# Kernel optimization log

Measured on AMD Instinct MI355X. Metric: run time of the kernel, lower is better.

## Reference

```python
import jax, jax.numpy as jnp
import numpy as np

B, S, T = 256, 1024, 64

def setup_inputs() -> dict:
    key = jax.random.key(0)
    k1, k2, k3, k4, k5 = jax.random.split(key, 5)
    emissions = jax.random.normal(k1, (B, S, T), dtype=jnp.float32)
    tags = jax.random.randint(k2, (B, S), 0, T, dtype=jnp.int64)
    mask = jnp.ones((B, S), dtype=jnp.int32)
    transitions = jax.random.normal(k3, (T, T), dtype=jnp.float32) * 0.1
    start_transitions = jax.random.normal(k4, (T,), dtype=jnp.float32) * 0.1
    end_transitions = jax.random.normal(k5, (T,), dtype=jnp.float32) * 0.1
    return {"emissions": emissions, "tags": tags, "mask": mask,
            "transitions": transitions, "start_transitions": start_transitions,
            "end_transitions": end_transitions}


def _gold_score(emissions, tags, maskf, transitions, start_transitions, end_transitions):
    # emission score at each gold tag: [B, S]
    emit = jnp.take_along_axis(emissions, tags[:, :, None], axis=2)[:, :, 0]
    # transition score between consecutive gold tags: [B, S-1]
    trans = transitions[tags[:, :-1], tags[:, 1:]]
    score = start_transitions[tags[:, 0]] + emit[:, 0]
    score = score + jnp.sum((trans + emit[:, 1:]) * maskf[:, 1:], axis=1)
    last_pos = maskf.astype(jnp.int32).sum(axis=1) - 1           # [B]
    last_tags = jnp.take_along_axis(tags, last_pos[:, None], axis=1)[:, 0]
    return score + end_transitions[last_tags]


def _log_partition(emissions, maskf, transitions, start_transitions, end_transitions):
    alpha0 = start_transitions[None, :] + emissions[:, 0]        # [B, T]

    def step(alpha, xs):
        emit_t, m_t = xs                                         # [B, T], [B]
        # scores[b, i, j] = alpha[b, i] + transitions[i, j] + emit_t[b, j]
        scores = alpha[:, :, None] + transitions[None, :, :] + emit_t[:, None, :]
        new_alpha = jax.nn.logsumexp(scores, axis=1)             # [B, T]
        alpha = jnp.where(m_t[:, None] > 0, new_alpha, alpha)
        return alpha, None

    xs = (jnp.swapaxes(emissions[:, 1:], 0, 1), jnp.swapaxes(maskf[:, 1:], 0, 1))
    alpha, _ = jax.lax.scan(step, alpha0, xs)
    return jax.nn.logsumexp(alpha + end_transitions[None, :], axis=1)  # [B]


def reference(emissions, tags, mask, transitions, start_transitions, end_transitions):
    maskf = mask.astype(emissions.dtype)
    log_Z = _log_partition(emissions, maskf, transitions, start_transitions, end_transitions)
    score = _gold_score(emissions, tags, maskf, transitions, start_transitions, end_transitions)
    return jnp.mean(log_Z - score)
```

## Files before the change

### kernel.cpp

```cpp
#include <hip/hip_runtime.h>

#define Bn 256
#define Sn 1024
#define Tn 64
#define NCH 16
#define BURN 64
#define SLAB 4
#define RAWSTR 260
#define CROW 72
#define MROW 129
#define LN2 0.69314718055994531f
#define L7LN2 4.8520302639196169f

typedef __attribute__((ext_vector_type(8))) short short8;
typedef __attribute__((ext_vector_type(4))) float f32x4;

__device__ __forceinline__ unsigned short f2bf_rne(float f) {
  unsigned u = __float_as_uint(f);
  u = (u + 0x7fffu + ((u >> 16) & 1u)) >> 16;
  return (unsigned short)u;
}
__device__ __forceinline__ unsigned pk2(float hi, float lo) {
  return __builtin_amdgcn_perm(__float_as_uint(hi), __float_as_uint(lo), 0x07060302);
}
__device__ __forceinline__ unsigned pke(float a, float b) {
  return (unsigned)f2bf_rne(__expf(a - L7LN2)) |
         ((unsigned)f2bf_rne(__expf(b - L7LN2)) << 16);
}
__device__ __forceinline__ short8 cat4(uint2 a, uint2 b) {
  union { unsigned u[4]; short8 s; } x;
  x.u[0] = a.x; x.u[1] = a.y; x.u[2] = b.x; x.u[3] = b.y;
  return x.s;
}
__device__ __forceinline__ void gl_lds16(const void* src, void* dst) {
  __builtin_amdgcn_global_load_lds(
      (const __attribute__((address_space(1))) void*)src,
      (__attribute__((address_space(3))) void*)dst, 16, 0, 0);
}
__device__ __forceinline__ void gl_lds4(const void* src, void* dst) {
  __builtin_amdgcn_global_load_lds(
      (const __attribute__((address_space(1))) void*)src,
      (__attribute__((address_space(3))) void*)dst, 4, 0, 0);
}

__global__ __launch_bounds__(128, 1) void crf_scan(
    const float* __restrict__ em, const int* __restrict__ tags,
    const int* __restrict__ mask, const float* __restrict__ trans,
    const float* __restrict__ startt, const float* __restrict__ endt,
    float* __restrict__ wsL, float* __restrict__ wsGold,
    int* __restrict__ wsM, float* __restrict__ wsSE, float* __restrict__ wsA,
    int* __restrict__ cnt, float* __restrict__ out) {
  const int g = blockIdx.x & 15;
  const int c = blockIdx.x >> 4;
  const int Wc = (c == 0) ? 0 : BURN;
  const int Lc = (c == NCH - 1) ? 63 : 64;
  const int TOT = Wc + Lc;
  const int NSLAB = (TOT + SLAB - 1) / SLAB;
  const int t0 = 64 * c + 1;
  const int tstart = t0 - Wc;
  const int tid = threadIdx.x;
  const int wid = tid >> 6;
  const int lane = tid & 63;
  const int m = lane & 15;
  const int q = lane >> 4;
  const int mrow = 8 * (m >> 2) + (m & 3);

  __shared__ __align__(16) float rawS[3][16 * RAWSTR];
  __shared__ __align__(16) short convS[2][SLAB * 16 * CROW];
  __shared__ int maskL[16 * MROW];
  __shared__ int lastF;
  __shared__ float eend[64];
  __shared__ float rsum[2];

  short8 a00, a01, a10, a11, a20, a21, a30, a31;
  uint2 st0, st1, st2, st3;
  float Slog = 0.f;
  int K = 0, NL = 0;
  const f32x4 zero4 = {0.f, 0.f, 0.f, 0.f};

  auto issue_slab = [&](int s) {
    if (s >= NSLAB) return;
    float* dstb = rawS[s % 3];
    const int rem = TOT - 4 * s;
    if (rem >= SLAB) {
      for (int mm = 0; mm < 16; ++mm)
        gl_lds16(em + ((size_t)(16 * g + mm) * Sn + tstart + 4 * s) * 64 + lane * 4,
                 dstb + mm * RAWSTR);
    } else {
      for (int mm = 0; mm < 16; ++mm)
        for (int u = 0; u < rem; ++u)
          gl_lds4(em + ((size_t)(16 * g + mm) * Sn + tstart + 4 * s + u) * 64 + lane,
                  dstb + mm * RAWSTR + u * 64);
    }
  };
  auto conv_u = [&](const float* rp, short* cb, int mm, int base, int u) {
    float4 v0 = *(const float4*)(rp + u * 64 + 0);
    float4 v1 = *(const float4*)(rp + u * 64 + 4);
    float4 v2 = *(const float4*)(rp + u * 64 + 8);
    float4 v3 = *(const float4*)(rp + u * 64 + 12);
    uint4 o0, o1;
    o0.x = pke(v0.x, v0.y); o0.y = pke(v0.z, v0.w);
    o1.x = pke(v1.x, v1.y); o1.y = pke(v1.z, v1.w);
    o0.z = pke(v2.x, v2.y); o0.w = pke(v2.z, v2.w);
    o1.z = pke(v3.x, v3.y); o1.w = pke(v3.z, v3.w);
    short* cw = cb + (u * 16 + mm) * CROW + base;
    *(uint4*)(cw) = o0;
    *(uint4*)(cw + 16) = o1;
  };
  auto convert_full = [&](int s) {
    const int mm = lane & 15, seg = lane >> 4;
    const float* rp = rawS[s % 3] + mm * RAWSTR + seg * 16;
    short* cb = convS[s & 1];
    const int base = (seg >> 1) * 32 + (seg & 1) * 8;
    #pragma unroll
    for (int u = 0; u < SLAB; ++u) conv_u(rp, cb, mm, base, u);
  };
  auto convert_tail = [&](int s) {
    if (s >= NSLAB) return;
    const int mm = lane & 15, seg = lane >> 4;
    const float* rp = rawS[s % 3] + mm * RAWSTR + seg * 16;
    short* cb = convS[s & 1];
    const int base = (seg >> 1) * 32 + (seg & 1) * 8;
    const int vu = min(SLAB, TOT - 4 * s);
    for (int u = 0; u < vu; ++u) conv_u(rp, cb, mm, base, u);
  };

  if (wid == 0) {
#define LOADA(tm, kc, dst) { \
    _Pragma("unroll") for (int jj = 0; jj < 8; ++jj) { \
      int kk = kc * 32 + q * 8 + jj; \
      dst[jj] = (short)f2bf_rne(__expf(trans[kk * Tn + (32 * ((tm) >> 1) + 4 * ((tm) & 1) + mrow)])); \
    } }
    LOADA(0, 0, a00) LOADA(0, 1, a01) LOADA(1, 0, a10) LOADA(1, 1, a11)
    LOADA(2, 0, a20) LOADA(2, 1, a21) LOADA(3, 0, a30) LOADA(3, 1, a31)
#undef LOADA
    if (c == 0) {
#define INIT0(off, ss) { \
      float4 sv = *(const float4*)(startt + (off)); \
      float4 ev = *(const float4*)(em + (size_t)(16 * g + m) * Sn * Tn + (off)); \
      ss.x = (unsigned)f2bf_rne(__expf(sv.x + ev.x)) | \
             ((unsigned)f2bf_rne(__expf(sv.y + ev.y)) << 16); \
      ss.y = (unsigned)f2bf_rne(__expf(sv.z + ev.z)) | \
             ((unsigned)f2bf_rne(__expf(sv.w + ev.w)) << 16); }
      INIT0(8 * q, st0) INIT0(8 * q + 4, st1)
      INIT0(32 + 8 * q, st2) INIT0(36 + 8 * q, st3)
#undef INIT0
    } else {
      st0.x = 0x3F803F80u; st0.y = 0x3F803F80u; st1 = st0; st2 = st0; st3 = st0;
    }
    issue_slab(0);
    issue_slab(1);
    asm volatile("s_waitcnt vmcnt(0)" ::: "memory");
  } else {
    for (int mm = 0; mm < 16; ++mm) {
      gl_lds4(mask + (size_t)(16 * g + mm) * Sn + tstart + lane,
              (void*)(maskL + mm * MROW));
      bool special = (c == NCH - 1) && (g == 15) && (mm == 15);
      if (!special)
        gl_lds4(mask + (size_t)(16 * g + mm) * Sn + tstart + 64 + lane,
                (void*)(maskL + mm * MROW + 64));
    }
    {
      const int bm = 16 * g + m;
      const int qq = q;
      const int* tg = tags + (size_t)bm * Sn;
      const int* mkb = mask + (size_t)bm * Sn;
      const float* emb = em + (size_t)bm * Sn * Tn;
      float acc = 0.f;
      int cntg = 0;
      #pragma unroll 4
      for (int i = 0; i < 16; ++i) {
        int t = t0 + qq + 4 * i;
        bool ok = t < t0 + Lc;
        int ts = ok ? t : t0;
        int mv = mkb[ts];
        int tp = tg[ts - 1], tc = tg[ts];
        float w = trans[tp * Tn + tc] + emb[(size_t)ts * Tn + tc];
        acc += (ok && mv) ? w : 0.f;
        cntg += ok ? mv : 0;
      }
      acc += __shfl_xor(acc, 16); acc += __shfl_xor(acc, 32);
      cntg += __shfl_xor(cntg, 16); cntg += __shfl_xor(cntg, 32);
      if (qq == 0) { wsGold[c * 256 + bm] = acc; wsM[c * 256 + bm] = cntg; }
    }
    if (c == NCH - 1 && g == 15) {
      int t = tstart + 64 + lane;
      if (t < Sn) maskL[15 * MROW + 64 + lane] = mask[(size_t)255 * Sn + t];
    }
    asm volatile("s_waitcnt vmcnt(0) lgkmcnt(0)" ::: "memory");
  }
  __syncthreads();

  if (wid == 0) {
    issue_slab(2);
    asm volatile("s_waitcnt vmcnt(0)" ::: "memory");
  } else {
    convert_full(0);
    asm volatile("s_waitcnt lgkmcnt(0)" ::: "memory");
  }
  __syncthreads();

#define UNP(ss, x0, x1, x2, x3) \
  x0 = __uint_as_float(ss.x << 16); x1 = __uint_as_float(ss.x & 0xffff0000u); \
  x2 = __uint_as_float(ss.y << 16); x3 = __uint_as_float(ss.y & 0xffff0000u);

  auto renorm = [&](int ttz) {
    float x00, x01, x02, x03, x10, x11, x12, x13;
    float x20, x21, x22, x23, x30, x31, x32, x33;
    UNP(st0, x00, x01, x02, x03) UNP(st1, x10, x11, x12, x13)
    UNP(st2, x20, x21, x22, x23) UNP(st3, x30, x31, x32, x33)
    float sm = (((x00 + x01) + (x02 + x03)) + ((x10 + x11) + (x12 + x13)))
             + (((x20 + x21) + (x22 + x23)) + ((x30 + x31) + (x32 + x33)));
    sm += __shfl_xor(sm, 16); sm += __shfl_xor(sm, 32);
    if (c != 0 && ttz == BURN) { Slog = __logf(sm); K = 0; NL = 0; }
    int k = 127 - (int)((__float_as_uint(sm) >> 23) & 255u);
    float fk = __uint_as_float((unsigned)(127 + k) << 23);
    x00 *= fk; x01 *= fk; x02 *= fk; x03 *= fk;
    x10 *= fk; x11 *= fk; x12 *= fk; x13 *= fk;
    x20 *= fk; x21 *= fk; x22 *= fk; x23 *= fk;
    x30 *= fk; x31 *= fk; x32 *= fk; x33 *= fk;
    st0.x = pk2(x01, x00); st0.y = pk2(x03, x02);
    st1.x = pk2(x11, x10); st1.y = pk2(x13, x12);
    st2.x = pk2(x21, x20); st2.y = pk2(x23, x22);
    st3.x = pk2(x31, x30); st3.y = pk2(x33, x32);
    K += k;
  };

  auto scan_step = [&](const short* ep, int tt) {
    uint2 eu0 = *(const uint2*)(ep + 0 + 4 * q);
    uint2 eu1 = *(const uint2*)(ep + 16 + 4 * q);
    uint2 eu2 = *(const uint2*)(ep + 32 + 4 * q);
    uint2 eu3 = *(const uint2*)(ep + 48 + 4 * q);
    int mv = maskL[m * MROW + tt];
    short8 b0 = cat4(st0, st1);
    short8 b1 = cat4(st2, st3);
    f32x4 d0 = __builtin_amdgcn_mfma_f32_16x16x32_bf16(a00, b0, zero4, 0, 0, 0);
    f32x4 d1 = __builtin_amdgcn_mfma_f32_16x16x32_bf16(a10, b0, zero4, 0, 0, 0);
    f32x4 d2 = __builtin_amdgcn_mfma_f32_16x16x32_bf16(a20, b0, zero4, 0, 0, 0);
    f32x4 d3 = __builtin_amdgcn_mfma_f32_16x16x32_bf16(a30, b0, zero4, 0, 0, 0);
    d0 = __builtin_amdgcn_mfma_f32_16x16x32_bf16(a01, b1, d0, 0, 0, 0);
    d1 = __builtin_amdgcn_mfma_f32_16x16x32_bf16(a11, b1, d1, 0, 0, 0);
    d2 = __builtin_amdgcn_mfma_f32_16x16x32_bf16(a21, b1, d2, 0, 0, 0);
    d3 = __builtin_amdgcn_mfma_f32_16x16x32_bf16(a31, b1, d3, 0, 0, 0);
    const bool live = (mv != 0);
#define EPI(dd, eu, ss) { \
    float e0 = __uint_as_float(eu.x << 16); \
    float e1 = __uint_as_float(eu.x & 0xffff0000u); \
    float e2 = __uint_as_float(eu.y << 16); \
    float e3 = __uint_as_float(eu.y & 0xffff0000u); \
    unsigned nx = pk2(dd[1] * e1, dd[0] * e0); \
    unsigned ny = pk2(dd[3] * e3, dd[2] * e2); \
    ss.x = live ? nx : ss.x; \
    ss.y = live ? ny : ss.y; }
    EPI(d0, eu0, st0) EPI(d1, eu1, st1) EPI(d2, eu2, st2) EPI(d3, eu3, st3)
#undef EPI
    NL += (live && tt >= Wc) ? 1 : 0;
  };

  const int RT = (TOT - 4) >> 2;
  for (int r = 0; r < NSLAB; ++r) {
    if (wid == 0) {
      issue_slab(r + 3);
      if ((r & 1) == 0) renorm(4 * r);
      const short* cbase = convS[r & 1];
      if (r < RT) {
        #pragma unroll
        for (int u = 0; u < SLAB; ++u)
          scan_step(cbase + (u * 16 + m) * CROW, 4 * r + u);
      } else {
        #pragma unroll
        for (int u = 0; u < SLAB; ++u)
          if (4 * r + u < TOT)
            scan_step(cbase + (u * 16 + m) * CROW, 4 * r + u);
      }
      if (r + 3 < NSLAB) asm volatile("s_waitcnt vmcnt(16)" ::: "memory");
      else               asm volatile("s_waitcnt vmcnt(0)" ::: "memory");
    } else {
      if (r < RT) convert_full(r + 1);
      else        convert_tail(r + 1);
      asm volatile("s_waitcnt lgkmcnt(0)" ::: "memory");
    }
    __builtin_amdgcn_s_barrier();
    asm volatile("" ::: "memory");
  }

  if (wid == 0) {
    float x00, x01, x02, x03, x10, x11, x12, x13;
    float x20, x21, x22, x23, x30, x31, x32, x33;
    UNP(st0, x00, x01, x02, x03) UNP(st1, x10, x11, x12, x13)
    UNP(st2, x20, x21, x22, x23) UNP(st3, x30, x31, x32, x33)
    float sm = (((x00 + x01) + (x02 + x03)) + ((x10 + x11) + (x12 + x13)))
             + (((x20 + x21) + (x22 + x23)) + ((x30 + x31) + (x32 + x33)));
    sm += __shfl_xor(sm, 16); sm += __shfl_xor(sm, 32);
    const int bm = 16 * g + m;
    float L = __logf(sm) - Slog + LN2 * (float)(7 * NL - K);
    if (q == 0) wsL[c * 256 + bm] = L;
    if (c == NCH - 1) {
      if (q == 0) wsSE[bm] = __logf(sm);
      wsA[(8 * q + 0) * 256 + bm] = x00;  wsA[(8 * q + 1) * 256 + bm] = x01;
      wsA[(8 * q + 2) * 256 + bm] = x02;  wsA[(8 * q + 3) * 256 + bm] = x03;
      wsA[(8 * q + 4) * 256 + bm] = x10;  wsA[(8 * q + 5) * 256 + bm] = x11;
      wsA[(8 * q + 6) * 256 + bm] = x12;  wsA[(8 * q + 7) * 256 + bm] = x13;
      wsA[(32 + 8 * q + 0) * 256 + bm] = x20; wsA[(32 + 8 * q + 1) * 256 + bm] = x21;
      wsA[(32 + 8 * q + 2) * 256 + bm] = x22; wsA[(32 + 8 * q + 3) * 256 + bm] = x23;
      wsA[(36 + 8 * q + 0) * 256 + bm] = x30; wsA[(36 + 8 * q + 1) * 256 + bm] = x31;
      wsA[(36 + 8 * q + 2) * 256 + bm] = x32; wsA[(36 + 8 * q + 3) * 256 + bm] = x33;
    }
  }
#undef UNP

  __threadfence();
  __syncthreads();
  if (tid == 0) lastF = (atomicAdd(cnt, 1) == 255) ? 1 : 0;
  __syncthreads();
  if (lastF) {
    __threadfence();
    if (tid < 64) eend[tid] = __expf(endt[tid]);
    __syncthreads();
    float vsum = 0.f;
    for (int bb = tid; bb < Bn; bb += 128) {
      float sumL = 0.f, gold = 0.f;
      int msum = 0;
      #pragma unroll
      for (int cc = 0; cc < NCH; ++cc) {
        sumL += wsL[cc * 256 + bb];
        gold += wsGold[cc * 256 + bb];
        msum += wsM[cc * 256 + bb];
      }
      msum += mask[(size_t)bb * Sn];
      float se = 0.f;
      for (int jj = 0; jj < Tn; ++jj) se += wsA[jj * 256 + bb] * eend[jj];
      float logZ = sumL + __logf(se) - wsSE[bb];
      int tg0 = tags[(size_t)bb * Sn];
      int lastTag = tags[(size_t)bb * Sn + (msum - 1)];
      gold += startt[tg0] + em[(size_t)bb * Sn * Tn + tg0] + endt[lastTag];
      vsum += logZ - gold;
    }
    #pragma unroll
    for (int o = 32; o > 0; o >>= 1) vsum += __shfl_xor(vsum, o, 64);
    if (lane == 0) rsum[wid] = vsum;
    __syncthreads();
    if (tid == 0) out[0] = (rsum[0] + rsum[1]) * (1.0f / Bn);
  }
}

extern "C" void kernel_launch(void* const* d_in, const int* in_sizes, int n_in,
                              void* d_out, int out_size, void* d_ws, size_t ws_size,
                              hipStream_t stream) {
  const float* em     = (const float*)d_in[0];
  const int*   tags   = (const int*)d_in[1];
  const int*   mask   = (const int*)d_in[2];
  const float* trans  = (const float*)d_in[3];
  const float* startt = (const float*)d_in[4];
  const float* endt   = (const float*)d_in[5];
  float* out = (float*)d_out;

  float* wsL    = (float*)d_ws;
  float* wsGold = wsL + NCH * 256;
  int*   wsM    = (int*)(wsGold + NCH * 256);
  float* wsSE   = (float*)(wsM + NCH * 256);
  float* wsA    = wsSE + 256;
  int*   cnt    = (int*)(wsA + 64 * 256);

  hipMemsetAsync(cnt, 0, sizeof(int), stream);
  crf_scan<<<256, 128, 0, stream>>>(em, tags, mask, trans, startt, endt,
                                    wsL, wsGold, wsM, wsSE, wsA, cnt, out);
}
```

Before: 169.5 us.

## Split CRF scan block into four specialized waves for load, convert and scan

Raises the block from 2 to 4 wavefronts. Wave 0 only runs the MFMA scan, wave 3 issues the global-to-LDS slab loads, and waves 1 and 2 each convert half of every slab to bf16. The raw buffer goes from triple to double buffering because prefetch now runs one slab ahead on its own wave. The aim is to take load issue and conversion off the scan wave's critical path, at the cost of full __syncthreads per slab across more waves and a shallower prefetch depth.

```diff
diff --git a/kernel.cpp b/kernel.cpp
--- a/kernel.cpp
+++ b/kernel.cpp
@@ -43,7 +43,7 @@
       (__attribute__((address_space(3))) void*)dst, 4, 0, 0);
 }
 
-__global__ __launch_bounds__(128, 1) void crf_scan(
+__global__ __launch_bounds__(256, 1) void crf_scan(
     const float* __restrict__ em, const int* __restrict__ tags,
     const int* __restrict__ mask, const float* __restrict__ trans,
     const float* __restrict__ startt, const float* __restrict__ endt,
@@ -65,12 +65,12 @@
   const int q = lane >> 4;
   const int mrow = 8 * (m >> 2) + (m & 3);
 
-  __shared__ __align__(16) float rawS[3][16 * RAWSTR];
+  __shared__ __align__(16) float rawS[2][16 * RAWSTR];
   __shared__ __align__(16) short convS[2][SLAB * 16 * CROW];
   __shared__ int maskL[16 * MROW];
   __shared__ int lastF;
   __shared__ float eend[64];
-  __shared__ float rsum[2];
+  __shared__ float rsum[4];
 
   short8 a00, a01, a10, a11, a20, a21, a30, a31;
   uint2 st0, st1, st2, st3;
@@ -80,7 +80,7 @@
 
   auto issue_slab = [&](int s) {
     if (s >= NSLAB) return;
-    float* dstb = rawS[s % 3];
+    float* dstb = rawS[s & 1];
     const int rem = TOT - 4 * s;
     if (rem >= SLAB) {
       for (int mm = 0; mm < 16; ++mm)
@@ -107,22 +107,23 @@
     *(uint4*)(cw) = o0;
     *(uint4*)(cw + 16) = o1;
   };
-  auto convert_full = [&](int s) {
+  auto convert2 = [&](int s, int ua) {
     const int mm = lane & 15, seg = lane >> 4;
-    const float* rp = rawS[s % 3] + mm * RAWSTR + seg * 16;
+    const float* rp = rawS[s & 1] + mm * RAWSTR + seg * 16;
     short* cb = convS[s & 1];
     const int base = (seg >> 1) * 32 + (seg & 1) * 8;
-    #pragma unroll
-    for (int u = 0; u < SLAB; ++u) conv_u(rp, cb, mm, base, u);
-  };
-  auto convert_tail = [&](int s) {
+    conv_u(rp, cb, mm, base, ua);
+    conv_u(rp, cb, mm, base, ua + 1);
+  };
+  auto convert_tail2 = [&](int s, int ua) {
     if (s >= NSLAB) return;
     const int mm = lane & 15, seg = lane >> 4;
-    const float* rp = rawS[s % 3] + mm * RAWSTR + seg * 16;
+    const float* rp = rawS[s & 1] + mm * RAWSTR + seg * 16;
     short* cb = convS[s & 1];
     const int base = (seg >> 1) * 32 + (seg & 1) * 8;
     const int vu = min(SLAB, TOT - 4 * s);
-    for (int u = 0; u < vu; ++u) conv_u(rp, cb, mm, base, u);
+    const int ub = min(vu, ua + 2);
+    for (int u = ua; u < ub; ++u) conv_u(rp, cb, mm, base, u);
   };
 
   if (wid == 0) {
@@ -148,10 +149,7 @@
     } else {
       st0.x = 0x3F803F80u; st0.y = 0x3F803F80u; st1 = st0; st2 = st0; st3 = st0;
     }
-    issue_slab(0);
-    issue_slab(1);
-    asm volatile("s_waitcnt vmcnt(0)" ::: "memory");
-  } else {
+  } else if (wid == 1) {
     for (int mm = 0; mm < 16; ++mm) {
       gl_lds4(mask + (size_t)(16 * g + mm) * Sn + tstart + lane,
               (void*)(maskL + mm * MROW));
@@ -160,44 +158,42 @@
         gl_lds4(mask + (size_t)(16 * g + mm) * Sn + tstart + 64 + lane,
                 (void*)(maskL + mm * MROW + 64));
     }
-    {
-      const int bm = 16 * g + m;
-      const int qq = q;
-      const int* tg = tags + (size_t)bm * Sn;
-      const int* mkb = mask + (size_t)bm * Sn;
-      const float* emb = em + (size_t)bm * Sn * Tn;
-      float acc = 0.f;
-      int cntg = 0;
-      #pragma unroll 4
-      for (int i = 0; i < 16; ++i) {
-        int t = t0 + qq + 4 * i;
-        bool ok = t < t0 + Lc;
-        int ts = ok ? t : t0;
-        int mv = mkb[ts];
-        int tp = tg[ts - 1], tc = tg[ts];
-        float w = trans[tp * Tn + tc] + emb[(size_t)ts * Tn + tc];
-        acc += (ok && mv) ? w : 0.f;
-        cntg += ok ? mv : 0;
-      }
-      acc += __shfl_xor(acc, 16); acc += __shfl_xor(acc, 32);
-      cntg += __shfl_xor(cntg, 16); cntg += __shfl_xor(cntg, 32);
-      if (qq == 0) { wsGold[c * 256 + bm] = acc; wsM[c * 256 + bm] = cntg; }
-    }
     if (c == NCH - 1 && g == 15) {
       int t = tstart + 64 + lane;
       if (t < Sn) maskL[15 * MROW + 64 + lane] = mask[(size_t)255 * Sn + t];
     }
     asm volatile("s_waitcnt vmcnt(0) lgkmcnt(0)" ::: "memory");
+  } else if (wid == 2) {
+    const int bm = 16 * g + m;
+    const int qq = q;
+    const int* tg = tags + (size_t)bm * Sn;
+    const int* mkb = mask + (size_t)bm * Sn;
+    const float* emb = em + (size_t)bm * Sn * Tn;
+    float acc = 0.f;
+    int cntg = 0;
+    #pragma unroll 4
+    for (int i = 0; i < 16; ++i) {
+      int t = t0 + qq + 4 * i;
+      bool ok = t < t0 + Lc;
+      int ts = ok ? t : t0;
+      int mv = mkb[ts];
+      int tp = tg[ts - 1], tc = tg[ts];
+      float w = trans[tp * Tn + tc] + emb[(size_t)ts * Tn + tc];
+      acc += (ok && mv) ? w : 0.f;
+      cntg += ok ? mv : 0;
+    }
+    acc += __shfl_xor(acc, 16); acc += __shfl_xor(acc, 32);
+    cntg += __shfl_xor(cntg, 16); cntg += __shfl_xor(cntg, 32);
+    if (qq == 0) { wsGold[c * 256 + bm] = acc; wsM[c * 256 + bm] = cntg; }
+  } else {
+    issue_slab(0);
+    issue_slab(1);
+    asm volatile("s_waitcnt vmcnt(0)" ::: "memory");
   }
   __syncthreads();
 
-  if (wid == 0) {
-    issue_slab(2);
-    asm volatile("s_waitcnt vmcnt(0)" ::: "memory");
-  } else {
-    convert_full(0);
-    asm volatile("s_waitcnt lgkmcnt(0)" ::: "memory");
-  }
+  if (wid == 1) convert2(0, 0);
+  else if (wid == 2) convert2(0, 2);
   __syncthreads();
 
 #define UNP(ss, x0, x1, x2, x3) \
@@ -260,7 +256,6 @@
   const int RT = (TOT - 4) >> 2;
   for (int r = 0; r < NSLAB; ++r) {
     if (wid == 0) {
-      issue_slab(r + 3);
       if ((r & 1) == 0) renorm(4 * r);
       const short* cbase = convS[r & 1];
       if (r < RT) {
@@ -273,15 +268,15 @@
           if (4 * r + u < TOT)
             scan_step(cbase + (u * 16 + m) * CROW, 4 * r + u);
       }
-      if (r + 3 < NSLAB) asm volatile("s_waitcnt vmcnt(16)" ::: "memory");
-      else               asm volatile("s_waitcnt vmcnt(0)" ::: "memory");
+    } else if (wid == 3) {
+      issue_slab(r + 2);
+      asm volatile("s_waitcnt vmcnt(0)" ::: "memory");
     } else {
-      if (r < RT) convert_full(r + 1);
-      else        convert_tail(r + 1);
-      asm volatile("s_waitcnt lgkmcnt(0)" ::: "memory");
-    }
-    __builtin_amdgcn_s_barrier();
-    asm volatile("" ::: "memory");
+      const int ua = (wid == 1) ? 0 : 2;
+      if (r < RT) convert2(r + 1, ua);
+      else        convert_tail2(r + 1, ua);
+    }
+    __syncthreads();
   }
 
   if (wid == 0) {
@@ -318,7 +313,7 @@
     if (tid < 64) eend[tid] = __expf(endt[tid]);
     __syncthreads();
     float vsum = 0.f;
-    for (int bb = tid; bb < Bn; bb += 128) {
+    for (int bb = tid; bb < Bn; bb += 256) {
       float sumL = 0.f, gold = 0.f;
       int msum = 0;
       #pragma unroll
@@ -340,7 +335,7 @@
     for (int o = 32; o > 0; o >>= 1) vsum += __shfl_xor(vsum, o, 64);
     if (lane == 0) rsum[wid] = vsum;
     __syncthreads();
-    if (tid == 0) out[0] = (rsum[0] + rsum[1]) * (1.0f / Bn);
+    if (tid == 0) out[0] = (rsum[0] + rsum[1] + rsum[2] + rsum[3]) * (1.0f / Bn);
   }
 }
 
@@ -363,6 +358,6 @@
   int*   cnt    = (int*)(wsA + 64 * 256);
 
   hipMemsetAsync(cnt, 0, sizeof(int), stream);
-  crf_scan<<<256, 128, 0, stream>>>(em, tags, mask, trans, startt, endt,
+  crf_scan<<<256, 256, 0, stream>>>(em, tags, mask, trans, startt, endt,
                                     wsL, wsGold, wsM, wsSE, wsA, cnt, out);
 }
```

New measurement: 163.1 us. 1.04x faster.

## Collapse producer/consumer wavefronts into a single wave with inline emission conversion

Applied to the files above, without the earlier changes.

Drops the second wavefront that converted raw emissions to bf16 exp values in LDS. The single scan wave now reads raw fp32 slabs directly and does the exp/bf16 packing inline in each step, using a 4-deep raw slab ring with vmcnt-based waits. This removes the per-slab workgroup barriers and the convert-buffer LDS traffic. In exchange, the exp work and the gold-score/mask prologue now sit on the serial critical path of the one remaining wave.

```diff
diff --git a/kernel.cpp b/kernel.cpp
--- a/kernel.cpp
+++ b/kernel.cpp
@@ -7,7 +7,6 @@
 #define BURN 64
 #define SLAB 4
 #define RAWSTR 260
-#define CROW 72
 #define MROW 129
 #define LN2 0.69314718055994531f
 #define L7LN2 4.8520302639196169f
@@ -43,7 +42,7 @@
       (__attribute__((address_space(3))) void*)dst, 4, 0, 0);
 }
 
-__global__ __launch_bounds__(128, 1) void crf_scan(
+__global__ __launch_bounds__(64, 1) void crf_scan(
     const float* __restrict__ em, const int* __restrict__ tags,
     const int* __restrict__ mask, const float* __restrict__ trans,
     const float* __restrict__ startt, const float* __restrict__ endt,
@@ -58,19 +57,13 @@
   const int NSLAB = (TOT + SLAB - 1) / SLAB;
   const int t0 = 64 * c + 1;
   const int tstart = t0 - Wc;
-  const int tid = threadIdx.x;
-  const int wid = tid >> 6;
-  const int lane = tid & 63;
+  const int lane = threadIdx.x & 63;
   const int m = lane & 15;
   const int q = lane >> 4;
   const int mrow = 8 * (m >> 2) + (m & 3);
 
-  __shared__ __align__(16) float rawS[3][16 * RAWSTR];
-  __shared__ __align__(16) short convS[2][SLAB * 16 * CROW];
+  __shared__ __align__(16) float rawS[4][16 * RAWSTR];
   __shared__ int maskL[16 * MROW];
-  __shared__ int lastF;
-  __shared__ float eend[64];
-  __shared__ float rsum[2];
 
   short8 a00, a01, a10, a11, a20, a21, a30, a31;
   uint2 st0, st1, st2, st3;
@@ -80,7 +73,7 @@
 
   auto issue_slab = [&](int s) {
     if (s >= NSLAB) return;
-    float* dstb = rawS[s % 3];
+    float* dstb = rawS[s & 3];
     const int rem = TOT - 4 * s;
     if (rem >= SLAB) {
       for (int mm = 0; mm < 16; ++mm)
@@ -93,112 +86,68 @@
                   dstb + mm * RAWSTR + u * 64);
     }
   };
-  auto conv_u = [&](const float* rp, short* cb, int mm, int base, int u) {
-    float4 v0 = *(const float4*)(rp + u * 64 + 0);
-    float4 v1 = *(const float4*)(rp + u * 64 + 4);
-    float4 v2 = *(const float4*)(rp + u * 64 + 8);
-    float4 v3 = *(const float4*)(rp + u * 64 + 12);
-    uint4 o0, o1;
-    o0.x = pke(v0.x, v0.y); o0.y = pke(v0.z, v0.w);
-    o1.x = pke(v1.x, v1.y); o1.y = pke(v1.z, v1.w);
-    o0.z = pke(v2.x, v2.y); o0.w = pke(v2.z, v2.w);
-    o1.z = pke(v3.x, v3.y); o1.w = pke(v3.z, v3.w);
-    short* cw = cb + (u * 16 + mm) * CROW + base;
-    *(uint4*)(cw) = o0;
-    *(uint4*)(cw + 16) = o1;
-  };
-  auto convert_full = [&](int s) {
-    const int mm = lane & 15, seg = lane >> 4;
-    const float* rp = rawS[s % 3] + mm * RAWSTR + seg * 16;
-    short* cb = convS[s & 1];
-    const int base = (seg >> 1) * 32 + (seg & 1) * 8;
-    #pragma unroll
-    for (int u = 0; u < SLAB; ++u) conv_u(rp, cb, mm, base, u);
-  };
-  auto convert_tail = [&](int s) {
-    if (s >= NSLAB) return;
-    const int mm = lane & 15, seg = lane >> 4;
-    const float* rp = rawS[s % 3] + mm * RAWSTR + seg * 16;
-    short* cb = convS[s & 1];
-    const int base = (seg >> 1) * 32 + (seg & 1) * 8;
-    const int vu = min(SLAB, TOT - 4 * s);
-    for (int u = 0; u < vu; ++u) conv_u(rp, cb, mm, base, u);
-  };
-
-  if (wid == 0) {
+
+  for (int mm = 0; mm < 16; ++mm) {
+    gl_lds4(mask + (size_t)(16 * g + mm) * Sn + tstart + lane,
+            (void*)(maskL + mm * MROW));
+    bool special = (c == NCH - 1) && (g == 15) && (mm == 15);
+    if (!special)
+      gl_lds4(mask + (size_t)(16 * g + mm) * Sn + tstart + 64 + lane,
+              (void*)(maskL + mm * MROW + 64));
+  }
+  issue_slab(0); issue_slab(1); issue_slab(2);
+
 #define LOADA(tm, kc, dst) { \
     _Pragma("unroll") for (int jj = 0; jj < 8; ++jj) { \
       int kk = kc * 32 + q * 8 + jj; \
       dst[jj] = (short)f2bf_rne(__expf(trans[kk * Tn + (32 * ((tm) >> 1) + 4 * ((tm) & 1) + mrow)])); \
     } }
-    LOADA(0, 0, a00) LOADA(0, 1, a01) LOADA(1, 0, a10) LOADA(1, 1, a11)
-    LOADA(2, 0, a20) LOADA(2, 1, a21) LOADA(3, 0, a30) LOADA(3, 1, a31)
+  LOADA(0, 0, a00) LOADA(0, 1, a01) LOADA(1, 0, a10) LOADA(1, 1, a11)
+  LOADA(2, 0, a20) LOADA(2, 1, a21) LOADA(3, 0, a30) LOADA(3, 1, a31)
 #undef LOADA
-    if (c == 0) {
+
+  if (c == 0) {
 #define INIT0(off, ss) { \
-      float4 sv = *(const float4*)(startt + (off)); \
-      float4 ev = *(const float4*)(em + (size_t)(16 * g + m) * Sn * Tn + (off)); \
-      ss.x = (unsigned)f2bf_rne(__expf(sv.x + ev.x)) | \
-             ((unsigned)f2bf_rne(__expf(sv.y + ev.y)) << 16); \
-      ss.y = (unsigned)f2bf_rne(__expf(sv.z + ev.z)) | \
-             ((unsigned)f2bf_rne(__expf(sv.w + ev.w)) << 16); }
-      INIT0(8 * q, st0) INIT0(8 * q + 4, st1)
-      INIT0(32 + 8 * q, st2) INIT0(36 + 8 * q, st3)
+    float4 sv = *(const float4*)(startt + (off)); \
+    float4 ev = *(const float4*)(em + (size_t)(16 * g + m) * Sn * Tn + (off)); \
+    ss.x = (unsigned)f2bf_rne(__expf(sv.x + ev.x)) | \
+           ((unsigned)f2bf_rne(__expf(sv.y + ev.y)) << 16); \
+    ss.y = (unsigned)f2bf_rne(__expf(sv.z + ev.z)) | \
+           ((unsigned)f2bf_rne(__expf(sv.w + ev.w)) << 16); }
+    INIT0(8 * q, st0) INIT0(8 * q + 4, st1)
+    INIT0(32 + 8 * q, st2) INIT0(36 + 8 * q, st3)
 #undef INIT0
-    } else {
-      st0.x = 0x3F803F80u; st0.y = 0x3F803F80u; st1 = st0; st2 = st0; st3 = st0;
-    }
-    issue_slab(0);
-    issue_slab(1);
-    asm volatile("s_waitcnt vmcnt(0)" ::: "memory");
   } else {
-    for (int mm = 0; mm < 16; ++mm) {
-      gl_lds4(mask + (size_t)(16 * g + mm) * Sn + tstart + lane,
-              (void*)(maskL + mm * MROW));
-      bool special = (c == NCH - 1) && (g == 15) && (mm == 15);
-      if (!special)
-        gl_lds4(mask + (size_t)(16 * g + mm) * Sn + tstart + 64 + lane,
-                (void*)(maskL + mm * MROW + 64));
-    }
-    {
-      const int bm = 16 * g + m;
-      const int qq = q;
-      const int* tg = tags + (size_t)bm * Sn;
-      const int* mkb = mask + (size_t)bm * Sn;
-      const float* emb = em + (size_t)bm * Sn * Tn;
-      float acc = 0.f;
-      int cntg = 0;
-      #pragma unroll 4
-      for (int i = 0; i < 16; ++i) {
-        int t = t0 + qq + 4 * i;
-        bool ok = t < t0 + Lc;
-        int ts = ok ? t : t0;
-        int mv = mkb[ts];
-        int tp = tg[ts - 1], tc = tg[ts];
-        float w = trans[tp * Tn + tc] + emb[(size_t)ts * Tn + tc];
-        acc += (ok && mv) ? w : 0.f;
-        cntg += ok ? mv : 0;
-      }
-      acc += __shfl_xor(acc, 16); acc += __shfl_xor(acc, 32);
-      cntg += __shfl_xor(cntg, 16); cntg += __shfl_xor(cntg, 32);
-      if (qq == 0) { wsGold[c * 256 + bm] = acc; wsM[c * 256 + bm] = cntg; }
-    }
-    if (c == NCH - 1 && g == 15) {
-      int t = tstart + 64 + lane;
-      if (t < Sn) maskL[15 * MROW + 64 + lane] = mask[(size_t)255 * Sn + t];
-    }
-    asm volatile("s_waitcnt vmcnt(0) lgkmcnt(0)" ::: "memory");
-  }
-  __syncthreads();
-
-  if (wid == 0) {
-    issue_slab(2);
-    asm volatile("s_waitcnt vmcnt(0)" ::: "memory");
-  } else {
-    convert_full(0);
-    asm volatile("s_waitcnt lgkmcnt(0)" ::: "memory");
-  }
-  __syncthreads();
+    st0.x = 0x3F803F80u; st0.y = 0x3F803F80u; st1 = st0; st2 = st0; st3 = st0;
+  }
+
+  {
+    const int bm = 16 * g + m;
+    const int* tg = tags + (size_t)bm * Sn;
+    const int* mkb = mask + (size_t)bm * Sn;
+    const float* emb = em + (size_t)bm * Sn * Tn;
+    float acc = 0.f;
+    int cntg = 0;
+    #pragma unroll 4
+    for (int i = 0; i < 16; ++i) {
+      int t = t0 + q + 4 * i;
+      bool ok = t < t0 + Lc;
+      int ts = ok ? t : t0;
+      int mv = mkb[ts];
+      int tp = tg[ts - 1], tc = tg[ts];
+      float w = trans[tp * Tn + tc] + emb[(size_t)ts * Tn + tc];
+      acc += (ok && mv) ? w : 0.f;
+      cntg += ok ? mv : 0;
+    }
+    acc += __shfl_xor(acc, 16); acc += __shfl_xor(acc, 32);
+    cntg += __shfl_xor(cntg, 16); cntg += __shfl_xor(cntg, 32);
+    if (q == 0) { wsGold[c * 256 + bm] = acc; wsM[c * 256 + bm] = cntg; }
+  }
+  if (c == NCH - 1 && g == 15) {
+    int t = tstart + 64 + lane;
+    if (t < Sn) maskL[15 * MROW + 64 + lane] = mask[(size_t)255 * Sn + t];
+  }
+  asm volatile("s_waitcnt vmcnt(0) lgkmcnt(0)" ::: "memory");
 
 #define UNP(ss, x0, x1, x2, x3) \
   x0 = __uint_as_float(ss.x << 16); x1 = __uint_as_float(ss.x & 0xffff0000u); \
@@ -226,11 +175,16 @@
     K += k;
   };
 
-  auto scan_step = [&](const short* ep, int tt) {
-    uint2 eu0 = *(const uint2*)(ep + 0 + 4 * q);
-    uint2 eu1 = *(const uint2*)(ep + 16 + 4 * q);
-    uint2 eu2 = *(const uint2*)(ep + 32 + 4 * q);
-    uint2 eu3 = *(const uint2*)(ep + 48 + 4 * q);
+  auto scan_step = [&](const float* rp, int tt) {
+    float4 vA = *(const float4*)(rp + 8 * q);
+    float4 vB = *(const float4*)(rp + 8 * q + 4);
+    float4 vC = *(const float4*)(rp + 32 + 8 * q);
+    float4 vD = *(const float4*)(rp + 36 + 8 * q);
+    uint2 eu0, eu1, eu2, eu3;
+    eu0.x = pke(vA.x, vA.y); eu0.y = pke(vA.z, vA.w);
+    eu1.x = pke(vB.x, vB.y); eu1.y = pke(vB.z, vB.w);
+    eu2.x = pke(vC.x, vC.y); eu2.y = pke(vC.z, vC.w);
+    eu3.x = pke(vD.x, vD.y); eu3.y = pke(vD.z, vD.w);
     int mv = maskL[m * MROW + tt];
     short8 b0 = cat4(st0, st1);
     short8 b1 = cat4(st2, st3);
@@ -259,32 +213,24 @@
 
   const int RT = (TOT - 4) >> 2;
   for (int r = 0; r < NSLAB; ++r) {
-    if (wid == 0) {
-      issue_slab(r + 3);
-      if ((r & 1) == 0) renorm(4 * r);
-      const short* cbase = convS[r & 1];
-      if (r < RT) {
-        #pragma unroll
-        for (int u = 0; u < SLAB; ++u)
-          scan_step(cbase + (u * 16 + m) * CROW, 4 * r + u);
-      } else {
-        #pragma unroll
-        for (int u = 0; u < SLAB; ++u)
-          if (4 * r + u < TOT)
-            scan_step(cbase + (u * 16 + m) * CROW, 4 * r + u);
-      }
-      if (r + 3 < NSLAB) asm volatile("s_waitcnt vmcnt(16)" ::: "memory");
-      else               asm volatile("s_waitcnt vmcnt(0)" ::: "memory");
+    if ((r & 1) == 0) renorm(4 * r);
+    const float* rbase = rawS[r & 3] + m * RAWSTR;
+    if (r < RT) {
+      #pragma unroll
+      for (int u = 0; u < SLAB; ++u)
+        scan_step(rbase + u * 64, 4 * r + u);
     } else {
-      if (r < RT) convert_full(r + 1);
-      else        convert_tail(r + 1);
-      asm volatile("s_waitcnt lgkmcnt(0)" ::: "memory");
-    }
-    __builtin_amdgcn_s_barrier();
-    asm volatile("" ::: "memory");
-  }
-
-  if (wid == 0) {
+      #pragma unroll
+      for (int u = 0; u < SLAB; ++u)
+        if (4 * r + u < TOT)
+          scan_step(rbase + u * 64, 4 * r + u);
+    }
+    issue_slab(r + 3);
+    if (r + 4 <= NSLAB) asm volatile("s_waitcnt vmcnt(32)" ::: "memory");
+    else                asm volatile("s_waitcnt vmcnt(0)" ::: "memory");
+  }
+
+  {
     float x00, x01, x02, x03, x10, x11, x12, x13;
     float x20, x21, x22, x23, x30, x31, x32, x33;
     UNP(st0, x00, x01, x02, x03) UNP(st1, x10, x11, x12, x13)
@@ -310,15 +256,16 @@
 #undef UNP
 
   __threadfence();
-  __syncthreads();
-  if (tid == 0) lastF = (atomicAdd(cnt, 1) == 255) ? 1 : 0;
-  __syncthreads();
-  if (lastF) {
+  int last = 0;
+  if (lane == 0) last = (atomicAdd(cnt, 1) == 255) ? 1 : 0;
+  last = __shfl(last, 0, 64);
+  if (last) {
     __threadfence();
-    if (tid < 64) eend[tid] = __expf(endt[tid]);
-    __syncthreads();
+    float* eendL = rawS[0];
+    eendL[lane] = __expf(endt[lane]);
+    asm volatile("s_waitcnt lgkmcnt(0)" ::: "memory");
     float vsum = 0.f;
-    for (int bb = tid; bb < Bn; bb += 128) {
+    for (int bb = lane; bb < Bn; bb += 64) {
       float sumL = 0.f, gold = 0.f;
       int msum = 0;
       #pragma unroll
@@ -329,7 +276,7 @@
       }
       msum += mask[(size_t)bb * Sn];
       float se = 0.f;
-      for (int jj = 0; jj < Tn; ++jj) se += wsA[jj * 256 + bb] * eend[jj];
+      for (int jj = 0; jj < Tn; ++jj) se += wsA[jj * 256 + bb] * eendL[jj];
       float logZ = sumL + __logf(se) - wsSE[bb];
       int tg0 = tags[(size_t)bb * Sn];
       int lastTag = tags[(size_t)bb * Sn + (msum - 1)];
@@ -338,9 +285,7 @@
     }
     #pragma unroll
     for (int o = 32; o > 0; o >>= 1) vsum += __shfl_xor(vsum, o, 64);
-    if (lane == 0) rsum[wid] = vsum;
-    __syncthreads();
-    if (tid == 0) out[0] = (rsum[0] + rsum[1]) * (1.0f / Bn);
+    if (lane == 0) out[0] = vsum * (1.0f / Bn);
   }
 }
 
@@ -363,6 +308,6 @@
   int*   cnt    = (int*)(wsA + 64 * 256);
 
   hipMemsetAsync(cnt, 0, sizeof(int), stream);
-  crf_scan<<<256, 128, 0, stream>>>(em, tags, mask, trans, startt, endt,
-                                    wsL, wsGold, wsM, wsSE, wsA, cnt, out);
-}
+  crf_scan<<<256, 64, 0, stream>>>(em, tags, mask, trans, startt, endt,
+                                   wsL, wsGold, wsM, wsSE, wsA, cnt, out);
+}
```

Measured after the change: 182.0 us. +7.4%, slower.
